# Kernel optimization log

Hardware: AMD Instinct MI355X
Metric: run time of the kernel (lower is better)

The kernel has to match this reference:

```python
import jax, jax.numpy as jnp
import numpy as np

S = 7
B = 2
C = 20
COORD = 5.0
NOOBJ = 0.5
N_IMG = 16384
SS = S * S
F = B * 5 + C  # 30


def setup_inputs() -> dict:
    key = jax.random.key(0)
    k1, k2, k3, k4 = jax.random.split(key, 4)
    preds = jax.random.uniform(k1, (N_IMG, SS, F), dtype=jnp.float32)
    # targets built per the YOLOv1 encoding described in the docstring
    t_probs = jax.random.uniform(k2, (N_IMG, SS, C), dtype=jnp.float32)
    obj = jax.random.bernoulli(k3, 0.3, (N_IMG, SS))
    t_conf = jnp.where(obj[..., None], 1.0, -1.0) * jnp.ones((N_IMG, SS, B), jnp.float32)
    t_box = jax.random.uniform(k4, (N_IMG, SS, B * 4), dtype=jnp.float32,
                               minval=0.05, maxval=1.0)
    t_box = jnp.where(obj[..., None], t_box, 0.0)
    targets = jnp.concatenate([t_probs, t_conf, t_box], axis=-1)
    return {"preds": preds, "targets": targets}


def _iou(pb, tb):
    # pb, tb: (N, SS, B, 4) as (cx, cy, w, h) -> (N, SS, B)
    xA = jnp.maximum(pb[..., 0] - pb[..., 2] / 2, tb[..., 0] - tb[..., 2] / 2)
    yA = jnp.maximum(pb[..., 1] - pb[..., 3] / 2, tb[..., 1] - tb[..., 3] / 2)
    xB = jnp.minimum(pb[..., 0] + pb[..., 2] / 2, tb[..., 0] + tb[..., 2] / 2)
    yB = jnp.minimum(pb[..., 1] + pb[..., 3] / 2, tb[..., 1] + tb[..., 3] / 2)
    inter = jnp.maximum(0.0, xB - xA) * jnp.maximum(0.0, yB - yA)
    areaA = pb[..., 2] * pb[..., 3]
    areaB = tb[..., 2] * tb[..., 3]
    return inter / (areaA + areaB - inter)


def reference(preds, targets):
    N = preds.shape[0]
    p_probs = preds[..., :C]
    p_conf = preds[..., C:C + B]
    p_box = preds[..., C + B:].reshape(N, SS, B, 4)
    t_probs = targets[..., :C]
    t_conf = targets[..., C:C + B]
    t_box = targets[..., C + B:].reshape(N, SS, B, 4)

    obj = t_conf[..., 0] > 0  # (N, SS)

    # no-obj weighted confidence SSE over ALL cells (original adds it unconditionally)
    loss = NOOBJ * jnp.sum((p_conf - t_conf) ** 2)

    # class-prob SSE only at object cells
    loss = loss + jnp.sum(jnp.where(obj, jnp.sum((p_probs - t_probs) ** 2, axis=-1), 0.0))

    # IoU-based responsible-box selection (original computes IoU via numpy -> no grad)
    scores = jax.lax.stop_gradient(_iou(p_box, t_box))  # (N, SS, B)
    best = jnp.argmax(scores, axis=-1)  # (N, SS)

    # extra confidence term for the responsible box
    pc = jnp.take_along_axis(p_conf, best[..., None], axis=-1)[..., 0]
    tc = jnp.take_along_axis(t_conf, best[..., None], axis=-1)[..., 0]
    loss = loss + (1.0 - NOOBJ) * jnp.sum(jnp.where(obj, (pc - tc) ** 2, 0.0))

    # coordinate loss for the responsible box
    pb = jnp.take_along_axis(p_box, best[..., None, None], axis=-2)[..., 0, :]  # (N, SS, 4)
    tb = jnp.take_along_axis(t_box, best[..., None, None], axis=-2)[..., 0, :]
    # guard sqrt at no-obj cells (target w/h are 0 there; masked out of the loss)
    tb_wh = jnp.where(obj[..., None], tb[..., 2:4], 1.0)
    bl = ((pb[..., 0] - tb[..., 0]) ** 2
          + (pb[..., 1] - tb[..., 1]) ** 2
          + (jnp.sqrt(pb[..., 2]) - jnp.sqrt(tb_wh[..., 0])) ** 2
          + (jnp.sqrt(pb[..., 3]) - jnp.sqrt(tb_wh[..., 1])) ** 2)
    loss = loss + COORD * jnp.sum(jnp.where(obj, bl, 0.0))

    return loss / N
```

## Files before the change

### kernel.cpp

```cpp
#include <hip/hip_runtime.h>

#define S_      7
#define SS_     49
#define B_      2
#define C_      20
#define F_      30
#define N_IMG_  16384
#define NCELL_  (N_IMG_ * SS_)
#define COORD_  5.0f
#define NOOBJ_  0.5f

#define TPB           256
#define CELLS_PER_BLK TPB
#define NBLK          (NCELL_ / CELLS_PER_BLK)
#define FLT_PER_BLK   (CELLS_PER_BLK * F_)
#define VEC4_PER_BLK  (FLT_PER_BLK / 4)

typedef const __attribute__((address_space(1))) void g_void;
typedef __attribute__((address_space(3))) void lds_void;

__device__ __forceinline__ float iou_f(const float* pb, const float* tb) {
    float xA = fmaxf(pb[0] - pb[2] * 0.5f, tb[0] - tb[2] * 0.5f);
    float yA = fmaxf(pb[1] - pb[3] * 0.5f, tb[1] - tb[3] * 0.5f);
    float xB = fminf(pb[0] + pb[2] * 0.5f, tb[0] + tb[2] * 0.5f);
    float yB = fminf(pb[1] + pb[3] * 0.5f, tb[1] + tb[3] * 0.5f);
    float inter = fmaxf(0.f, xB - xA) * fmaxf(0.f, yB - yA);
    float areaA = pb[2] * pb[3];
    float areaB = tb[2] * tb[3];
    return inter / (areaA + areaB - inter);
}

__global__ __launch_bounds__(TPB) void mploss_kernel(
        const float* __restrict__ preds,
        const float* __restrict__ targets,
        float* __restrict__ part) {
    __shared__ alignas(16) float s_p[FLT_PER_BLK];
    __shared__ alignas(16) float s_t[FLT_PER_BLK];
    __shared__ float s_red[TPB / 64];

    const int tid  = threadIdx.x;
    const int lane = tid & 63;
    const int wave = tid >> 6;

    const float4* p4 = (const float4*)preds   + (long)blockIdx.x * VEC4_PER_BLK;
    const float4* t4 = (const float4*)targets + (long)blockIdx.x * VEC4_PER_BLK;

    for (int c = wave; c < 30; c += 4) {
        __builtin_amdgcn_global_load_lds(
            (g_void*)(p4 + c * 64 + lane),
            (lds_void*)(s_p + c * 256), 16, 0, 0);
        __builtin_amdgcn_global_load_lds(
            (g_void*)(t4 + c * 64 + lane),
            (lds_void*)(s_t + c * 256), 16, 0, 0);
    }
    __syncthreads();

    const float* p = s_p + tid * F_;
    const float* q = s_t + tid * F_;

    float l = 0.f;

    {
        float d0 = p[20] - q[20];
        float d1 = p[21] - q[21];
        l += NOOBJ_ * (d0 * d0 + d1 * d1);
    }

    const bool obj = q[20] > 0.f;
    if (obj) {
        float sprob = 0.f;
        #pragma unroll
        for (int f = 0; f < C_; ++f) {
            float d = p[f] - q[f];
            sprob += d * d;
        }
        l += sprob;

        float i0 = iou_f(p + 22, q + 22);
        float i1 = iou_f(p + 26, q + 26);
        int best = (i1 > i0) ? 1 : 0;

        float dc = p[20 + best] - q[20 + best];
        l += (1.0f - NOOBJ_) * dc * dc;

        const float* pb = p + 22 + 4 * best;
        const float* tb = q + 22 + 4 * best;
        float bx = pb[0] - tb[0];
        float by = pb[1] - tb[1];
        float bw = sqrtf(pb[2]) - sqrtf(tb[2]);
        float bh = sqrtf(pb[3]) - sqrtf(tb[3]);
        l += COORD_ * (bx * bx + by * by + bw * bw + bh * bh);
    }

    #pragma unroll
    for (int off = 32; off > 0; off >>= 1)
        l += __shfl_down(l, off, 64);

    if (lane == 0) s_red[wave] = l;
    __syncthreads();
    if (tid == 0)
        part[blockIdx.x] = s_red[0] + s_red[1] + s_red[2] + s_red[3];
}

__global__ __launch_bounds__(TPB) void reduce_kernel(
        const float* __restrict__ part, float* __restrict__ out) {
    __shared__ float s_red[TPB / 64];
    float v = 0.f;
    for (int i = threadIdx.x; i < NBLK; i += TPB) v += part[i];
    #pragma unroll
    for (int off = 32; off > 0; off >>= 1)
        v += __shfl_down(v, off, 64);
    const int wave = threadIdx.x >> 6;
    const int lane = threadIdx.x & 63;
    if (lane == 0) s_red[wave] = v;
    __syncthreads();
    if (threadIdx.x == 0)
        out[0] = (s_red[0] + s_red[1] + s_red[2] + s_red[3]) * (1.0f / (float)N_IMG_);
}

extern "C" void kernel_launch(void* const* d_in, const int* in_sizes, int n_in,
                              void* d_out, int out_size, void* d_ws, size_t ws_size,
                              hipStream_t stream) {
    const float* preds   = (const float*)d_in[0];
    const float* targets = (const float*)d_in[1];
    float* out  = (float*)d_out;
    float* part = (float*)d_ws;

    mploss_kernel<<<NBLK, TPB, 0, stream>>>(preds, targets, part);
    reduce_kernel<<<1, TPB, 0, stream>>>(part, out);
}
```

Measured before the change: 205.4 us.

## Use persistent blocks with register-prefetched tiles double-buffered into LDS

Replaces the one-tile-per-block grid (3136 blocks) with 512 persistent blocks that loop over tiles. Each wave loads half of one tensor's tile into registers, prefetching the next tile while the current tile's loss is computed from LDS. The aim is to overlap global loads with compute and to cut block launch overhead. In exchange it uses 15 float4 registers per thread, adds two barriers per tile, and drops the async global-to-LDS load path.

```diff
diff --git a/kernel.cpp b/kernel.cpp
--- a/kernel.cpp
+++ b/kernel.cpp
@@ -1,23 +1,19 @@
 #include <hip/hip_runtime.h>
 
-#define S_      7
-#define SS_     49
-#define B_      2
-#define C_      20
 #define F_      30
 #define N_IMG_  16384
+#define SS_     49
 #define NCELL_  (N_IMG_ * SS_)
 #define COORD_  5.0f
 #define NOOBJ_  0.5f
 
-#define TPB           256
-#define CELLS_PER_BLK TPB
-#define NBLK          (NCELL_ / CELLS_PER_BLK)
-#define FLT_PER_BLK   (CELLS_PER_BLK * F_)
-#define VEC4_PER_BLK  (FLT_PER_BLK / 4)
-
-typedef const __attribute__((address_space(1))) void g_void;
-typedef __attribute__((address_space(3))) void lds_void;
+#define TPB             256
+#define CELLS_PER_TILE  256
+#define NTILE           (NCELL_ / CELLS_PER_TILE)
+#define NBLK_P          512
+#define FLT_PER_TILE    (CELLS_PER_TILE * F_)
+#define VEC4_PER_TILE   (FLT_PER_TILE / 4)
+#define K_SLOTS         15
 
 __device__ __forceinline__ float iou_f(const float* pb, const float* tb) {
     float xA = fmaxf(pb[0] - pb[2] * 0.5f, tb[0] - tb[2] * 0.5f);
@@ -30,47 +26,16 @@
     return inter / (areaA + areaB - inter);
 }
 
-__global__ __launch_bounds__(TPB) void mploss_kernel(
-        const float* __restrict__ preds,
-        const float* __restrict__ targets,
-        float* __restrict__ part) {
-    __shared__ alignas(16) float s_p[FLT_PER_BLK];
-    __shared__ alignas(16) float s_t[FLT_PER_BLK];
-    __shared__ float s_red[TPB / 64];
-
-    const int tid  = threadIdx.x;
-    const int lane = tid & 63;
-    const int wave = tid >> 6;
-
-    const float4* p4 = (const float4*)preds   + (long)blockIdx.x * VEC4_PER_BLK;
-    const float4* t4 = (const float4*)targets + (long)blockIdx.x * VEC4_PER_BLK;
-
-    for (int c = wave; c < 30; c += 4) {
-        __builtin_amdgcn_global_load_lds(
-            (g_void*)(p4 + c * 64 + lane),
-            (lds_void*)(s_p + c * 256), 16, 0, 0);
-        __builtin_amdgcn_global_load_lds(
-            (g_void*)(t4 + c * 64 + lane),
-            (lds_void*)(s_t + c * 256), 16, 0, 0);
-    }
-    __syncthreads();
-
-    const float* p = s_p + tid * F_;
-    const float* q = s_t + tid * F_;
-
-    float l = 0.f;
-
-    {
-        float d0 = p[20] - q[20];
-        float d1 = p[21] - q[21];
-        l += NOOBJ_ * (d0 * d0 + d1 * d1);
-    }
+__device__ __forceinline__ void cell_loss(float& l, const float* p, const float* q) {
+    float d0 = p[20] - q[20];
+    float d1 = p[21] - q[21];
+    l += NOOBJ_ * (d0 * d0 + d1 * d1);
 
     const bool obj = q[20] > 0.f;
     if (obj) {
         float sprob = 0.f;
         #pragma unroll
-        for (int f = 0; f < C_; ++f) {
+        for (int f = 0; f < 20; ++f) {
             float d = p[f] - q[f];
             sprob += d * d;
         }
@@ -91,11 +56,63 @@
         float bh = sqrtf(pb[3]) - sqrtf(tb[3]);
         l += COORD_ * (bx * bx + by * by + bw * bw + bh * bh);
     }
+}
+
+__global__ __launch_bounds__(TPB) void mploss_kernel(
+        const float* __restrict__ preds,
+        const float* __restrict__ targets,
+        float* __restrict__ part) {
+    __shared__ alignas(16) float s_p[FLT_PER_TILE];
+    __shared__ alignas(16) float s_t[FLT_PER_TILE];
+    __shared__ float s_red[TPB / 64];
+
+    const int tid  = threadIdx.x;
+    const int lane = tid & 63;
+    const int wave = tid >> 6;
+
+    const float4* g4   = (wave < 2) ? (const float4*)preds : (const float4*)targets;
+    float4*       lds4 = (wave < 2) ? (float4*)s_p : (float4*)s_t;
+    const int u0 = (wave & 1) * K_SLOTS;
+
+    float4 rv[K_SLOTS];
+
+    int t = blockIdx.x;
+    {
+        const long base = (long)t * VEC4_PER_TILE;
+        #pragma unroll
+        for (int k = 0; k < K_SLOTS; ++k)
+            rv[k] = g4[base + (u0 + k) * 64 + lane];
+        #pragma unroll
+        for (int k = 0; k < K_SLOTS; ++k)
+            lds4[(u0 + k) * 64 + lane] = rv[k];
+    }
+    __syncthreads();
+
+    float l = 0.f;
+    while (true) {
+        const int  tn        = t + NBLK_P;
+        const bool have_next = (tn < NTILE);
+        if (have_next) {
+            const long base = (long)tn * VEC4_PER_TILE;
+            #pragma unroll
+            for (int k = 0; k < K_SLOTS; ++k)
+                rv[k] = g4[base + (u0 + k) * 64 + lane];
+        }
+
+        cell_loss(l, s_p + tid * F_, s_t + tid * F_);
+
+        if (!have_next) break;
+        __syncthreads();
+        #pragma unroll
+        for (int k = 0; k < K_SLOTS; ++k)
+            lds4[(u0 + k) * 64 + lane] = rv[k];
+        __syncthreads();
+        t = tn;
+    }
 
     #pragma unroll
     for (int off = 32; off > 0; off >>= 1)
         l += __shfl_down(l, off, 64);
-
     if (lane == 0) s_red[wave] = l;
     __syncthreads();
     if (tid == 0)
@@ -106,7 +123,7 @@
         const float* __restrict__ part, float* __restrict__ out) {
     __shared__ float s_red[TPB / 64];
     float v = 0.f;
-    for (int i = threadIdx.x; i < NBLK; i += TPB) v += part[i];
+    for (int i = threadIdx.x; i < NBLK_P; i += TPB) v += part[i];
     #pragma unroll
     for (int off = 32; off > 0; off >>= 1)
         v += __shfl_down(v, off, 64);
@@ -126,6 +143,6 @@
     float* out  = (float*)d_out;
     float* part = (float*)d_ws;
 
-    mploss_kernel<<<NBLK, TPB, 0, stream>>>(preds, targets, part);
+    mploss_kernel<<<NBLK_P, TPB, 0, stream>>>(preds, targets, part);
     reduce_kernel<<<1, TPB, 0, stream>>>(part, out);
 }
```

New measurement: 237.2 us. 1.15x slower.

## Use persistent single-wave blocks looping over tiles with two cells per lane

Applied to the files above, without the earlier changes.

Replaces one 256-thread block per 256 cells with 1280 persistent 64-thread blocks. Each block loops over 128-cell tiles, loads them into LDS with global_load_lds, and each lane handles two cells. Block-level syncthreads are replaced by explicit s_waitcnt, and the per-block reduction becomes a single wave shuffle. This cuts block launch and sync overhead and shrinks the partial-sum array. The cost is no overlap between one tile's load and the next tile's compute, and fewer waves in flight to hide memory latency.

```diff
diff --git a/kernel.cpp b/kernel.cpp
--- a/kernel.cpp
+++ b/kernel.cpp
@@ -1,20 +1,19 @@
 #include <hip/hip_runtime.h>
 
-#define S_      7
-#define SS_     49
-#define B_      2
-#define C_      20
 #define F_      30
 #define N_IMG_  16384
+#define SS_     49
 #define NCELL_  (N_IMG_ * SS_)
 #define COORD_  5.0f
 #define NOOBJ_  0.5f
 
-#define TPB           256
-#define CELLS_PER_BLK TPB
-#define NBLK          (NCELL_ / CELLS_PER_BLK)
-#define FLT_PER_BLK   (CELLS_PER_BLK * F_)
-#define VEC4_PER_BLK  (FLT_PER_BLK / 4)
+#define TPB     64
+#define CPT     128
+#define TILE_F  (CPT * F_)
+#define TILE_B  (TILE_F * 4)
+#define NCHUNK  15
+#define NT      (NCELL_ / CPT)
+#define NB      1280
 
 typedef const __attribute__((address_space(1))) void g_void;
 typedef __attribute__((address_space(3))) void lds_void;
@@ -30,47 +29,16 @@
     return inter / (areaA + areaB - inter);
 }
 
-__global__ __launch_bounds__(TPB) void mploss_kernel(
-        const float* __restrict__ preds,
-        const float* __restrict__ targets,
-        float* __restrict__ part) {
-    __shared__ alignas(16) float s_p[FLT_PER_BLK];
-    __shared__ alignas(16) float s_t[FLT_PER_BLK];
-    __shared__ float s_red[TPB / 64];
-
-    const int tid  = threadIdx.x;
-    const int lane = tid & 63;
-    const int wave = tid >> 6;
-
-    const float4* p4 = (const float4*)preds   + (long)blockIdx.x * VEC4_PER_BLK;
-    const float4* t4 = (const float4*)targets + (long)blockIdx.x * VEC4_PER_BLK;
-
-    for (int c = wave; c < 30; c += 4) {
-        __builtin_amdgcn_global_load_lds(
-            (g_void*)(p4 + c * 64 + lane),
-            (lds_void*)(s_p + c * 256), 16, 0, 0);
-        __builtin_amdgcn_global_load_lds(
-            (g_void*)(t4 + c * 64 + lane),
-            (lds_void*)(s_t + c * 256), 16, 0, 0);
-    }
-    __syncthreads();
-
-    const float* p = s_p + tid * F_;
-    const float* q = s_t + tid * F_;
-
-    float l = 0.f;
-
-    {
-        float d0 = p[20] - q[20];
-        float d1 = p[21] - q[21];
-        l += NOOBJ_ * (d0 * d0 + d1 * d1);
-    }
+__device__ __forceinline__ void cell_loss(float& l, const float* p, const float* q) {
+    float d0 = p[20] - q[20];
+    float d1 = p[21] - q[21];
+    l += NOOBJ_ * (d0 * d0 + d1 * d1);
 
     const bool obj = q[20] > 0.f;
     if (obj) {
         float sprob = 0.f;
         #pragma unroll
-        for (int f = 0; f < C_; ++f) {
+        for (int f = 0; f < 20; ++f) {
             float d = p[f] - q[f];
             sprob += d * d;
         }
@@ -91,22 +59,57 @@
         float bh = sqrtf(pb[3]) - sqrtf(tb[3]);
         l += COORD_ * (bx * bx + by * by + bw * bw + bh * bh);
     }
+}
+
+__global__ __launch_bounds__(TPB) void mploss_kernel(
+        const float* __restrict__ preds,
+        const float* __restrict__ targets,
+        float* __restrict__ part) {
+    __shared__ alignas(16) float s_buf[2 * TILE_F];
+    float* const s_p = s_buf;
+    float* const s_t = s_buf + TILE_F;
+
+    const int lane = threadIdx.x;
+
+    const char* gp0 = (const char*)preds;
+    const char* gt0 = (const char*)targets;
+
+    float l = 0.f;
+
+    for (int t = blockIdx.x; t < NT; t += NB) {
+        {
+            const char* gp = gp0 + (size_t)t * TILE_B + lane * 16;
+            const char* gt = gt0 + (size_t)t * TILE_B + lane * 16;
+            #pragma unroll
+            for (int k = 0; k < NCHUNK; ++k) {
+                __builtin_amdgcn_global_load_lds(
+                    (g_void*)(gp + k * 1024),
+                    (lds_void*)((char*)s_p + k * 1024), 16, 0, 0);
+                __builtin_amdgcn_global_load_lds(
+                    (g_void*)(gt + k * 1024),
+                    (lds_void*)((char*)s_t + k * 1024), 16, 0, 0);
+            }
+        }
+        asm volatile("s_waitcnt vmcnt(0)" ::: "memory");
+
+        cell_loss(l, s_p + (2 * lane)     * F_, s_t + (2 * lane)     * F_);
+        cell_loss(l, s_p + (2 * lane + 1) * F_, s_t + (2 * lane + 1) * F_);
+
+        asm volatile("s_waitcnt lgkmcnt(0)" ::: "memory");
+    }
 
     #pragma unroll
     for (int off = 32; off > 0; off >>= 1)
         l += __shfl_down(l, off, 64);
-
-    if (lane == 0) s_red[wave] = l;
-    __syncthreads();
-    if (tid == 0)
-        part[blockIdx.x] = s_red[0] + s_red[1] + s_red[2] + s_red[3];
+    if (lane == 0)
+        part[blockIdx.x] = l;
 }
 
-__global__ __launch_bounds__(TPB) void reduce_kernel(
+__global__ __launch_bounds__(256) void reduce_kernel(
         const float* __restrict__ part, float* __restrict__ out) {
-    __shared__ float s_red[TPB / 64];
+    __shared__ float s_red[4];
     float v = 0.f;
-    for (int i = threadIdx.x; i < NBLK; i += TPB) v += part[i];
+    for (int i = threadIdx.x; i < NB; i += 256) v += part[i];
     #pragma unroll
     for (int off = 32; off > 0; off >>= 1)
         v += __shfl_down(v, off, 64);
@@ -126,6 +129,6 @@
     float* out  = (float*)d_out;
     float* part = (float*)d_ws;
 
-    mploss_kernel<<<NBLK, TPB, 0, stream>>>(preds, targets, part);
-    reduce_kernel<<<1, TPB, 0, stream>>>(part, out);
+    mploss_kernel<<<NB, TPB, 0, stream>>>(preds, targets, part);
+    reduce_kernel<<<1, 256, 0, stream>>>(part, out);
 }
```

Result: no change. 207.9 us (+1.2%).
